# Kernel tuning notes

Measured on AMD Instinct MI355X. Metric: run time of the kernel, lower is better.

## Reference

```python
import jax, jax.numpy as jnp
import numpy as np

B, H, W, C = 16, 56, 56, 256
K = 3          # ikernel
G = 8          # group
C4 = C // 4    # ratio=4
EPS = 1e-5


def setup_inputs() -> dict:
    key = jax.random.key(0)
    ks = jax.random.split(key, 16)
    s = lambda *sh: 1.0 / np.sqrt(sh[-1])
    inp = {
        'x': jax.random.normal(ks[0], (B, H, W, C), jnp.float32),
        # Involution: conv1 (C->C4, 1x1), BN affine, conv2 (C4 -> G*K*K, 1x1)
        'conv1_w': jax.random.normal(ks[1], (C4, C), jnp.float32) * s(C4, C),
        'conv1_b': jnp.zeros((C4,), jnp.float32),
        'bn_gamma': jnp.ones((C4,), jnp.float32),
        'bn_beta': jnp.zeros((C4,), jnp.float32),
        'conv2_w': jax.random.normal(ks[2], (G * K * K, C4), jnp.float32) * s(G * K * K, C4),
        'conv2_b': jnp.zeros((G * K * K,), jnp.float32),
        # mlp_c: Linear(dim, dim, bias=False)
        'mlp_c_w': jax.random.normal(ks[3], (C, C), jnp.float32) * s(C, C),
        # reweight1: Mlp(dim, dim//4, dim*2)
        'fc1_w': jax.random.normal(ks[4], (C4, C), jnp.float32) * s(C4, C),
        'fc1_b': jnp.zeros((C4,), jnp.float32),
        'fc2_w': jax.random.normal(ks[5], (2 * C, C4), jnp.float32) * s(2 * C, C4),
        'fc2_b': jnp.zeros((2 * C,), jnp.float32),
        # projcnn: Conv2d(dim, dim, 1)
        'projcnn_w': jax.random.normal(ks[6], (C, C), jnp.float32) * s(C, C),
        'projcnn_b': jnp.zeros((C,), jnp.float32),
    }
    return inp


def _involution(x, conv1_w, conv1_b, bn_gamma, bn_beta, conv2_w, conv2_b):
    # x: [B,H,W,C] (channels-last equivalent of the torch NCHW path)
    # kernel-generating branch: 1x1 conv -> BN (batch stats, training mode) -> relu -> 1x1 conv
    t = jnp.einsum('bhwc,oc->bhwo', x, conv1_w) + conv1_b          # [B,H,W,C4]
    mu = t.mean(axis=(0, 1, 2))
    var = t.var(axis=(0, 1, 2))
    t = jax.nn.relu(bn_gamma * (t - mu) * jax.lax.rsqrt(var + EPS) + bn_beta)
    w = jnp.einsum('bhwc,oc->bhwo', t, conv2_w) + conv2_b          # [B,H,W,G*K*K]
    w = w.reshape(B, H, W, G, K * K)
    # unfold: pad and stack the K*K shifted views (row-major kernel order, matches torch)
    p = K // 2
    xp = jnp.pad(x, ((0, 0), (p, p), (p, p), (0, 0)))
    patches = jnp.stack([xp[:, i:i + H, j:j + W, :] for i in range(K) for j in range(K)],
                        axis=3)                                     # [B,H,W,KK,C]
    patches = patches.reshape(B, H, W, K * K, G, C // G)
    out = jnp.einsum('bhwkgc,bhwgk->bhwgc', patches, w)             # multiply + sum over kernel dim
    return out.reshape(B, H, W, C)


def reference(x, conv1_w, conv1_b, bn_gamma, bn_beta, conv2_w, conv2_b,
              mlp_c_w, fc1_w, fc1_b, fc2_w, fc2_b, projcnn_w, projcnn_b):
    hw = _involution(x, conv1_w, conv1_b, bn_gamma, bn_beta, conv2_w, conv2_b)  # [B,H,W,C]
    c = jnp.einsum('bhwc,oc->bhwo', x, mlp_c_w)                                  # [B,H,W,C]
    a = (hw + c).mean(axis=(1, 2))                                               # [B,C]
    a = jax.nn.gelu(jnp.einsum('bc,oc->bo', a, fc1_w) + fc1_b, approximate=False)
    a = jnp.einsum('bc,oc->bo', a, fc2_w) + fc2_b                                # [B,2C]
    a = a.reshape(B, C, 2).transpose(2, 0, 1)                                    # [2,B,C]
    a = jax.nn.softmax(a, axis=0)[:, :, None, None, :]                           # [2,B,1,1,C]
    y = hw * a[0] + c * a[1]
    return jnp.einsum('bhwc,oc->bhwo', y, projcnn_w) + projcnn_b
```

## Files before the change

### kernel.cpp

```cpp
#include <hip/hip_runtime.h>
#include <math.h>

#define BB 16
#define HH 56
#define WW 56
#define CC 256
#define O2P 80
#define NPIX 50176
#define HWP 3136

typedef __attribute__((ext_vector_type(4))) float f32x4;
typedef __attribute__((ext_vector_type(8))) short bh8;
typedef __attribute__((ext_vector_type(4))) short bh4;

__device__ inline short f2bf(float f) {
    union { float f; unsigned u; } v; v.f = f;
    unsigned r = (v.u + 0x7fffu + ((v.u >> 16) & 1u)) >> 16;
    return (short)r;
}
__device__ inline float bf2f(short s) {
    union { unsigned u; float f; } v; v.u = ((unsigned)(unsigned short)s) << 16;
    return v.f;
}

__device__ inline void stage_tile(const short* __restrict__ src, int rowBase, int ldk,
                                  int kc, char* smem, int nchunks, int wid, int lane)
{
    for (int ci = wid; ci < nchunks; ci += 4) {
        int row = ci * 8 + (lane >> 3);
        int cb = (lane & 7) ^ (row & 7);
        const short* gp = src + (size_t)(rowBase + row) * ldk + kc + cb * 8;
        __builtin_amdgcn_global_load_lds(
            (const __attribute__((address_space(1))) void*)gp,
            (__attribute__((address_space(3))) void*)(smem + ci * 1024), 16, 0, 0);
    }
}

template<int BN, int AMODE, int OUTBF>
__global__ __launch_bounds__(256) void mgemm(
    const short* __restrict__ Ab,
    const short* __restrict__ At, const float* __restrict__ scsh,
    const short* __restrict__ Ah, const short* __restrict__ Ac,
    const float* __restrict__ g0, const float* __restrict__ g1,
    const short* __restrict__ Wb, const float* __restrict__ bias,
    void* __restrict__ outp, int K, int O, int ldOut)
{
    constexpr int WN = (BN == 128) ? 2 : 1;
    constexpr int MR = (BN == 128) ? 4 : 2;
    constexpr int NR = BN / (16 * WN);
    constexpr int BCH = BN / 8;

    __shared__ alignas(16) char smA[16384];
    __shared__ alignas(16) char smB[BN * 128];

    const int tid = threadIdx.x;
    const int lane = tid & 63, wid = tid >> 6;
    const int rowBase = blockIdx.x * 128;
    const int ocBase = blockIdx.y * BN;
    const int waveM = (BN == 128) ? (wid >> 1) * 64 : wid * 32;
    const int waveN = (BN == 128) ? (wid & 1) * 64 : 0;

    f32x4 acc[MR][NR];
    #pragma unroll
    for (int m = 0; m < MR; ++m)
        #pragma unroll
        for (int n = 0; n < NR; ++n) acc[m][n] = f32x4{0.f, 0.f, 0.f, 0.f};

    for (int kc = 0; kc < K; kc += 64) {
        if constexpr (AMODE == 0) {
            stage_tile(Ab, rowBase, K, kc, smA, 16, wid, lane);
        } else if constexpr (AMODE == 1) {
            #pragma unroll
            for (int q = tid; q < 1024; q += 256) {
                int row = q >> 3, cb = q & 7;
                bh8 v = *(const bh8*)(At + (size_t)(rowBase + row) * K + kc + cb * 8);
                bh8 o;
                #pragma unroll
                for (int j = 0; j < 8; ++j) {
                    int k = kc + cb * 8 + j;
                    o[j] = f2bf(fmaxf(bf2f(v[j]) * scsh[k] + scsh[64 + k], 0.f));
                }
                *(bh8*)(smA + row * 128 + ((cb ^ (row & 7)) << 4)) = o;
            }
        } else {
            #pragma unroll
            for (int q = tid; q < 1024; q += 256) {
                int row = q >> 3, cb = q & 7;
                int n = rowBase + row;
                int b = n / HWP;
                const size_t off = (size_t)n * 256 + kc + cb * 8;
                bh8 h8 = *(const bh8*)(Ah + off);
                bh8 c8 = *(const bh8*)(Ac + off);
                bh8 o;
                #pragma unroll
                for (int j = 0; j < 8; ++j) {
                    float w0 = g0[b * 256 + kc + cb * 8 + j];
                    float w1 = g1[b * 256 + kc + cb * 8 + j];
                    o[j] = f2bf(bf2f(h8[j]) * w0 + bf2f(c8[j]) * w1);
                }
                *(bh8*)(smA + row * 128 + ((cb ^ (row & 7)) << 4)) = o;
            }
        }
        stage_tile(Wb, ocBase, K, kc, smB, BCH, wid, lane);
        __syncthreads();

        #pragma unroll
        for (int ks = 0; ks < 2; ++ks) {
            bh8 aF[MR], bF[NR];
            #pragma unroll
            for (int m = 0; m < MR; ++m) {
                int r = waveM + m * 16 + (lane & 15);
                int cb = ks * 4 + (lane >> 4);
                aF[m] = *(const bh8*)(smA + r * 128 + ((cb ^ (r & 7)) << 4));
            }
            #pragma unroll
            for (int n = 0; n < NR; ++n) {
                int r = waveN + n * 16 + (lane & 15);
                int cb = ks * 4 + (lane >> 4);
                bF[n] = *(const bh8*)(smB + r * 128 + ((cb ^ (r & 7)) << 4));
            }
            #pragma unroll
            for (int m = 0; m < MR; ++m)
                #pragma unroll
                for (int n = 0; n < NR; ++n)
                    acc[m][n] = __builtin_amdgcn_mfma_f32_16x16x32_bf16(
                        aF[m], bF[n], acc[m][n], 0, 0, 0);
        }
        __syncthreads();
    }

    #pragma unroll
    for (int m = 0; m < MR; ++m)
        #pragma unroll
        for (int n = 0; n < NR; ++n)
            #pragma unroll
            for (int j = 0; j < 4; ++j) {
                int r = rowBase + waveM + m * 16 + (lane >> 4) * 4 + j;
                int c = ocBase + waveN + n * 16 + (lane & 15);
                if (c < O) {
                    float v = acc[m][n][j] + (bias ? bias[c] : 0.f);
                    if constexpr (OUTBF)
                        ((short*)outp)[(size_t)r * ldOut + c] = f2bf(v);
                    else
                        ((float*)outp)[(size_t)r * ldOut + c] = v;
                }
            }
}

__global__ __launch_bounds__(256) void cvt_x_kernel(const float* __restrict__ x,
                                                    short* __restrict__ xb,
                                                    float* __restrict__ sxb)
{
    __shared__ float sm[8][256];
    const int tid = threadIdx.x;
    size_t base = (size_t)blockIdx.x * 2048 + tid * 8;
    const int b = (int)(base >> 8) / HWP;
    const int ch0 = (int)(base & 255);
    const int pix = (tid * 8) >> 8;

    f32x4 v0 = *(const f32x4*)(x + base);
    f32x4 v1 = *(const f32x4*)(x + base + 4);
    bh8 o;
    #pragma unroll
    for (int j = 0; j < 4; ++j) { o[j] = f2bf(v0[j]); o[4 + j] = f2bf(v1[j]); }
    *(bh8*)(xb + base) = o;

    #pragma unroll
    for (int j = 0; j < 4; ++j) {
        sm[pix][ch0 + j] = v0[j];
        sm[pix][ch0 + 4 + j] = v1[j];
    }
    __syncthreads();
    float s = 0.f;
    #pragma unroll
    for (int p = 0; p < 8; ++p) s += sm[p][tid];
    atomicAdd(&sxb[b * CC + tid], s);
}

__global__ __launch_bounds__(256) void cvt_w_kernel(
    const float* __restrict__ c1, const float* __restrict__ mc,
    const float* __restrict__ pj, const float* __restrict__ c2,
    short* __restrict__ c1b, short* __restrict__ mcb,
    short* __restrict__ pjb, short* __restrict__ c2b)
{
    int i = blockIdx.x * 256 + threadIdx.x;
    if (i < 16384) c1b[i] = f2bf(c1[i]);
    if (i < 65536) { mcb[i] = f2bf(mc[i]); pjb[i] = f2bf(pj[i]); }
    if (i < O2P * 64) {
        int o = i >> 6, k = i & 63;
        c2b[i] = (o < 72) ? f2bf(c2[o * 64 + k]) : (short)0;
    }
}

__global__ __launch_bounds__(256) void bn_stats_kernel(
    const short* __restrict__ t, float* __restrict__ stats)
{
    __shared__ float ss[32][64], sq[32][64];
    const int tid = threadIdx.x;
    const int grp = tid >> 3, ch0 = (tid & 7) * 8;
    const size_t rowBase = (size_t)blockIdx.x * 512;
    float s[8] = {}, q[8] = {};
    for (int r = grp; r < 512; r += 32) {
        bh8 v = *(const bh8*)(t + (rowBase + r) * 64 + ch0);
        #pragma unroll
        for (int j = 0; j < 8; ++j) {
            float f = bf2f(v[j]);
            s[j] += f; q[j] += f * f;
        }
    }
    #pragma unroll
    for (int j = 0; j < 8; ++j) { ss[grp][ch0 + j] = s[j]; sq[grp][ch0 + j] = q[j]; }
    __syncthreads();
    if (tid < 64) {
        float ts = 0.f, tq = 0.f;
        #pragma unroll
        for (int g = 0; g < 32; ++g) { ts += ss[g][tid]; tq += sq[g][tid]; }
        atomicAdd(&stats[tid], ts);
        atomicAdd(&stats[64 + tid], tq);
    }
}

__global__ void bn_finalize_kernel(
    const float* __restrict__ stats, const float* __restrict__ gamma,
    const float* __restrict__ beta, float* __restrict__ scsh)
{
    int ch = threadIdx.x;
    const float invN = 1.f / (float)NPIX;
    float mean = stats[ch] * invN;
    float var  = stats[64 + ch] * invN - mean * mean;
    float sc = gamma[ch] * rsqrtf(var + 1e-5f);
    scsh[ch] = sc;
    scsh[64 + ch] = beta[ch] - mean * sc;
}

__global__ __launch_bounds__(256) void invol_kernel(
    const short* __restrict__ xb, const short* __restrict__ wmatb,
    short* __restrict__ hwb, float* __restrict__ asum)
{
    __shared__ float sm4[4][256];
    const int idx = blockIdx.x;
    const int s = idx & 1, bh = idx >> 1;
    const int b = bh / HH, h = bh % HH;
    const int tid = threadIdx.x;
    const int lane = tid & 63, wid = tid >> 6;
    const int c4 = lane * 4;
    const int g = lane >> 3;
    const int w0 = s * 28 + wid * 7;
    const short* xbase = xb + ((size_t)b * HWP) * CC + c4;

    float cL[3][4], cM[3][4], cR[3][4];
    auto loadcol = [&](int Wc, float d[3][4]) {
        #pragma unroll
        for (int i = 0; i < 3; ++i) {
            int hh = h + i - 1;
            if (Wc < 0 || Wc >= WW || hh < 0 || hh >= HH) {
                d[i][0] = d[i][1] = d[i][2] = d[i][3] = 0.f;
            } else {
                bh4 v = *(const bh4*)(xbase + (size_t)(hh * WW + Wc) * CC);
                #pragma unroll
                for (int j = 0; j < 4; ++j) d[i][j] = bf2f(v[j]);
            }
        }
    };
    loadcol(w0 - 1, cL);
    loadcol(w0, cM);

    float loc[4] = {0.f, 0.f, 0.f, 0.f};
    for (int w = w0; w < w0 + 7; ++w) {
        loadcol(w + 1, cR);
        const int n = bh * WW + w;
        const short* wr = wmatb + (size_t)n * O2P + g * 9;
        float wf[9];
        #pragma unroll
        for (int t9 = 0; t9 < 9; ++t9) wf[t9] = bf2f(wr[t9]);
        bh4 ov;
        #pragma unroll
        for (int j = 0; j < 4; ++j) {
            float a = cL[0][j] * wf[0] + cM[0][j] * wf[1] + cR[0][j] * wf[2]
                    + cL[1][j] * wf[3] + cM[1][j] * wf[4] + cR[1][j] * wf[5]
                    + cL[2][j] * wf[6] + cM[2][j] * wf[7] + cR[2][j] * wf[8];
            loc[j] += a;
            ov[j] = f2bf(a);
        }
        *(bh4*)(hwb + (size_t)n * CC + c4) = ov;
        #pragma unroll
        for (int i = 0; i < 3; ++i)
            #pragma unroll
            for (int j = 0; j < 4; ++j) { cL[i][j] = cM[i][j]; cM[i][j] = cR[i][j]; }
    }
    #pragma unroll
    for (int j = 0; j < 4; ++j) sm4[wid][c4 + j] = loc[j];
    __syncthreads();
    float tot = sm4[0][tid] + sm4[1][tid] + sm4[2][tid] + sm4[3][tid];
    atomicAdd(&asum[b * CC + tid], tot);
}

__global__ __launch_bounds__(256) void mlp_kernel(
    const float* __restrict__ asum, const float* __restrict__ sxb,
    const float* __restrict__ mlp_c_w,
    const float* __restrict__ fc1_w, const float* __restrict__ fc1_b,
    const float* __restrict__ fc2_w, const float* __restrict__ fc2_b,
    float* __restrict__ a0, float* __restrict__ a1)
{
    __shared__ float a[256], hbuf[64], f[512];
    const int b = blockIdx.x, tid = threadIdx.x;
    float acm = 0.f;
    const float* wrow = mlp_c_w + (size_t)tid * 256;
    for (int c = 0; c < 256; ++c) acm += sxb[b * CC + c] * wrow[c];
    a[tid] = (asum[b * CC + tid] + acm) * (1.f / (float)HWP);
    __syncthreads();
    if (tid < 64) {
        float s = fc1_b[tid];
        for (int c = 0; c < 256; ++c) s += a[c] * fc1_w[tid * 256 + c];
        hbuf[tid] = 0.5f * s * (1.f + erff(s * 0.7071067811865476f));
    }
    __syncthreads();
    for (int o = tid; o < 512; o += 256) {
        float s = fc2_b[o];
        for (int c = 0; c < 64; ++c) s += hbuf[c] * fc2_w[o * 64 + c];
        f[o] = s;
    }
    __syncthreads();
    float f0 = f[2 * tid], f1 = f[2 * tid + 1];
    float m = fmaxf(f0, f1);
    float e0 = expf(f0 - m), e1 = expf(f1 - m);
    float inv = 1.f / (e0 + e1);
    a0[b * CC + tid] = e0 * inv;
    a1[b * CC + tid] = e1 * inv;
}

extern "C" void kernel_launch(void* const* d_in, const int* in_sizes, int n_in,
                              void* d_out, int out_size, void* d_ws, size_t ws_size,
                              hipStream_t stream)
{
    (void)in_sizes; (void)n_in; (void)out_size; (void)ws_size;
    const float* x        = (const float*)d_in[0];
    const float* conv1_w  = (const float*)d_in[1];
    const float* conv1_b  = (const float*)d_in[2];
    const float* bn_gamma = (const float*)d_in[3];
    const float* bn_beta  = (const float*)d_in[4];
    const float* conv2_w  = (const float*)d_in[5];
    const float* conv2_b  = (const float*)d_in[6];
    const float* mlp_c_w  = (const float*)d_in[7];
    const float* fc1_w    = (const float*)d_in[8];
    const float* fc1_b    = (const float*)d_in[9];
    const float* fc2_w    = (const float*)d_in[10];
    const float* fc2_b    = (const float*)d_in[11];
    const float* projcnn_w= (const float*)d_in[12];
    const float* projcnn_b= (const float*)d_in[13];
    float* out = (float*)d_out;

    char* p = (char*)d_ws;
    short* xb  = (short*)p; p += (size_t)NPIX * 256 * 2;
    short* hwb = (short*)p; p += (size_t)NPIX * 256 * 2;
    short* cmb = (short*)p;
    short* t   = (short*)cmb;
    p += (size_t)NPIX * 256 * 2;
    short* wmatb = (short*)p; p += (size_t)NPIX * O2P * 2;
    short* c1b = (short*)p; p += 64 * 256 * 2;
    short* mcb = (short*)p; p += 256 * 256 * 2;
    short* pjb = (short*)p; p += 256 * 256 * 2;
    short* c2b = (short*)p; p += O2P * 64 * 2;
    float* stats = (float*)p; p += 128 * 4;
    float* asum  = (float*)p; p += BB * 256 * 4;
    float* sxb   = (float*)p; p += BB * 256 * 4;
    float* scsh  = (float*)p; p += 128 * 4;
    float* a0    = (float*)p; p += BB * 256 * 4;
    float* a1    = (float*)p; p += BB * 256 * 4;

    hipMemsetAsync(stats, 0, (128 + 2 * BB * 256) * sizeof(float), stream);

    cvt_x_kernel<<<NPIX * 256 / 2048, 256, 0, stream>>>(x, xb, sxb);
    cvt_w_kernel<<<256, 256, 0, stream>>>(conv1_w, mlp_c_w, projcnn_w, conv2_w,
                                          c1b, mcb, pjb, c2b);
    mgemm<64, 0, 1><<<dim3(392, 1), 256, 0, stream>>>(
        xb, nullptr, nullptr, nullptr, nullptr, nullptr, nullptr,
        c1b, conv1_b, t, 256, 64, 64);
    bn_stats_kernel<<<98, 256, 0, stream>>>(t, stats);
    bn_finalize_kernel<<<1, 64, 0, stream>>>(stats, bn_gamma, bn_beta, scsh);
    mgemm<O2P, 1, 1><<<dim3(392, 1), 256, 0, stream>>>(
        nullptr, t, scsh, nullptr, nullptr, nullptr, nullptr,
        c2b, conv2_b, wmatb, 64, 72, O2P);
    invol_kernel<<<BB * HH * 2, 256, 0, stream>>>(xb, wmatb, hwb, asum);
    mgemm<128, 0, 1><<<dim3(392, 2), 256, 0, stream>>>(
        xb, nullptr, nullptr, nullptr, nullptr, nullptr, nullptr,
        mcb, nullptr, cmb, 256, 256, 256);
    mlp_kernel<<<BB, 256, 0, stream>>>(asum, sxb, mlp_c_w,
                                       fc1_w, fc1_b, fc2_w, fc2_b, a0, a1);
    mgemm<128, 2, 0><<<dim3(392, 2), 256, 0, stream>>>(
        nullptr, nullptr, nullptr, hwb, cmb, a0, a1,
        pjb, projcnn_b, out, 256, 256, 256);
}
```

Baseline: 296.4 us.

## Fold softmax gates into per-batch projection weights and shrink GEMM row tiles

```diff
diff --git a/kernel.cpp b/kernel.cpp
--- a/kernel.cpp
+++ b/kernel.cpp
@@ -37,28 +37,29 @@
 }
 
 template<int BN, int AMODE, int OUTBF>
-__global__ __launch_bounds__(256) void mgemm(
-    const short* __restrict__ Ab,
-    const short* __restrict__ At, const float* __restrict__ scsh,
-    const short* __restrict__ Ah, const short* __restrict__ Ac,
-    const float* __restrict__ g0, const float* __restrict__ g1,
+__global__ __launch_bounds__(256) void mgemm64(
+    const short* __restrict__ Ab, const short* __restrict__ A2,
+    const float* __restrict__ scsh,
     const short* __restrict__ Wb, const float* __restrict__ bias,
     void* __restrict__ outp, int K, int O, int ldOut)
 {
-    constexpr int WN = (BN == 128) ? 2 : 1;
-    constexpr int MR = (BN == 128) ? 4 : 2;
-    constexpr int NR = BN / (16 * WN);
+    constexpr int MR = (BN == 80) ? 1 : 2;
+    constexpr int NR = (BN == 80) ? 5 : (BN == 128 ? 4 : 2);
     constexpr int BCH = BN / 8;
 
-    __shared__ alignas(16) char smA[16384];
+    __shared__ alignas(16) char smA[8192];
     __shared__ alignas(16) char smB[BN * 128];
 
     const int tid = threadIdx.x;
     const int lane = tid & 63, wid = tid >> 6;
-    const int rowBase = blockIdx.x * 128;
+    const int rowBase = blockIdx.x * 64;
     const int ocBase = blockIdx.y * BN;
-    const int waveM = (BN == 128) ? (wid >> 1) * 64 : wid * 32;
-    const int waveN = (BN == 128) ? (wid & 1) * 64 : 0;
+    const int waveM = (BN == 80) ? wid * 16 : (wid & 1) * 32;
+    const int waveN = (BN == 80) ? 0 : (BN == 128 ? (wid >> 1) * 64 : (wid >> 1) * 32);
+
+    const short* wptr = Wb;
+    if constexpr (AMODE == 3)
+        wptr += (size_t)(rowBase / HWP) * 256 * 512;
 
     f32x4 acc[MR][NR];
     #pragma unroll
@@ -68,12 +69,15 @@
 
     for (int kc = 0; kc < K; kc += 64) {
         if constexpr (AMODE == 0) {
-            stage_tile(Ab, rowBase, K, kc, smA, 16, wid, lane);
-        } else if constexpr (AMODE == 1) {
-            #pragma unroll
-            for (int q = tid; q < 1024; q += 256) {
+            stage_tile(Ab, rowBase, K, kc, smA, 8, wid, lane);
+        } else if constexpr (AMODE == 3) {
+            const short* s = (kc < 256) ? Ab : A2;
+            stage_tile(s, rowBase, 256, kc & 255, smA, 8, wid, lane);
+        } else {
+            #pragma unroll
+            for (int q = tid; q < 512; q += 256) {
                 int row = q >> 3, cb = q & 7;
-                bh8 v = *(const bh8*)(At + (size_t)(rowBase + row) * K + kc + cb * 8);
+                bh8 v = *(const bh8*)(Ab + (size_t)(rowBase + row) * K + kc + cb * 8);
                 bh8 o;
                 #pragma unroll
                 for (int j = 0; j < 8; ++j) {
@@ -82,26 +86,8 @@
                 }
                 *(bh8*)(smA + row * 128 + ((cb ^ (row & 7)) << 4)) = o;
             }
-        } else {
-            #pragma unroll
-            for (int q = tid; q < 1024; q += 256) {
-                int row = q >> 3, cb = q & 7;
-                int n = rowBase + row;
-                int b = n / HWP;
-                const size_t off = (size_t)n * 256 + kc + cb * 8;
-                bh8 h8 = *(const bh8*)(Ah + off);
-                bh8 c8 = *(const bh8*)(Ac + off);
-                bh8 o;
-                #pragma unroll
-                for (int j = 0; j < 8; ++j) {
-                    float w0 = g0[b * 256 + kc + cb * 8 + j];
-                    float w1 = g1[b * 256 + kc + cb * 8 + j];
-                    o[j] = f2bf(bf2f(h8[j]) * w0 + bf2f(c8[j]) * w1);
-                }
-                *(bh8*)(smA + row * 128 + ((cb ^ (row & 7)) << 4)) = o;
-            }
-        }
-        stage_tile(Wb, ocBase, K, kc, smB, BCH, wid, lane);
+        }
+        stage_tile(wptr, ocBase, K, kc, smB, BCH, wid, lane);
         __syncthreads();
 
         #pragma unroll
@@ -179,17 +165,32 @@
 
 __global__ __launch_bounds__(256) void cvt_w_kernel(
     const float* __restrict__ c1, const float* __restrict__ mc,
-    const float* __restrict__ pj, const float* __restrict__ c2,
-    short* __restrict__ c1b, short* __restrict__ mcb,
-    short* __restrict__ pjb, short* __restrict__ c2b)
+    const float* __restrict__ c2,
+    short* __restrict__ c1b, short* __restrict__ mcb, short* __restrict__ c2b)
 {
     int i = blockIdx.x * 256 + threadIdx.x;
     if (i < 16384) c1b[i] = f2bf(c1[i]);
-    if (i < 65536) { mcb[i] = f2bf(mc[i]); pjb[i] = f2bf(pj[i]); }
+    if (i < 65536) mcb[i] = f2bf(mc[i]);
     if (i < O2P * 64) {
         int o = i >> 6, k = i & 63;
         c2b[i] = (o < 72) ? f2bf(c2[o * 64 + k]) : (short)0;
     }
+}
+
+__global__ __launch_bounds__(256) void fold_w_kernel(
+    const float* __restrict__ pjw, const float* __restrict__ a0,
+    const float* __restrict__ a1, short* __restrict__ wf)
+{
+    size_t base = ((size_t)blockIdx.x * 256 + threadIdx.x) * 8;
+    int b = (int)(base >> 17);
+    int rem = (int)(base & 131071);
+    int o = rem >> 9, k0 = rem & 511;
+    const float* av = (k0 < 256) ? (a0 + b * 256 + k0) : (a1 + b * 256 + k0 - 256);
+    const float* wrow = pjw + o * 256 + (k0 & 255);
+    bh8 ov;
+    #pragma unroll
+    for (int j = 0; j < 8; ++j) ov[j] = f2bf(wrow[j] * av[j]);
+    *(bh8*)(wf + base) = ov;
 }
 
 __global__ __launch_bounds__(256) void bn_stats_kernel(
@@ -305,19 +306,36 @@
     __shared__ float a[256], hbuf[64], f[512];
     const int b = blockIdx.x, tid = threadIdx.x;
     float acm = 0.f;
-    const float* wrow = mlp_c_w + (size_t)tid * 256;
-    for (int c = 0; c < 256; ++c) acm += sxb[b * CC + c] * wrow[c];
+    {
+        const f32x4* w4 = (const f32x4*)(mlp_c_w + (size_t)tid * 256);
+        const f32x4* s4 = (const f32x4*)(sxb + b * CC);
+        for (int c = 0; c < 64; ++c) {
+            f32x4 sv = s4[c], wv = w4[c];
+            acm += sv[0] * wv[0] + sv[1] * wv[1] + sv[2] * wv[2] + sv[3] * wv[3];
+        }
+    }
     a[tid] = (asum[b * CC + tid] + acm) * (1.f / (float)HWP);
     __syncthreads();
     if (tid < 64) {
         float s = fc1_b[tid];
-        for (int c = 0; c < 256; ++c) s += a[c] * fc1_w[tid * 256 + c];
+        const f32x4* w4 = (const f32x4*)(fc1_w + (size_t)tid * 256);
+        const f32x4* a4 = (const f32x4*)a;
+        for (int c = 0; c < 64; ++c) {
+            f32x4 av = a4[c], wv = w4[c];
+            s += av[0] * wv[0] + av[1] * wv[1] + av[2] * wv[2] + av[3] * wv[3];
+        }
         hbuf[tid] = 0.5f * s * (1.f + erff(s * 0.7071067811865476f));
     }
     __syncthreads();
     for (int o = tid; o < 512; o += 256) {
         float s = fc2_b[o];
-        for (int c = 0; c < 64; ++c) s += hbuf[c] * fc2_w[o * 64 + c];
+        const f32x4* w4 = (const f32x4*)(fc2_w + (size_t)o * 64);
+        const f32x4* h4 = (const f32x4*)hbuf;
+        #pragma unroll
+        for (int c = 0; c < 16; ++c) {
+            f32x4 hv = h4[c], wv = w4[c];
+            s += hv[0] * wv[0] + hv[1] * wv[1] + hv[2] * wv[2] + hv[3] * wv[3];
+        }
         f[o] = s;
     }
     __syncthreads();
@@ -357,9 +375,9 @@
     short* t   = (short*)cmb;
     p += (size_t)NPIX * 256 * 2;
     short* wmatb = (short*)p; p += (size_t)NPIX * O2P * 2;
+    short* wfold = (short*)p; p += (size_t)BB * 256 * 512 * 2;
     short* c1b = (short*)p; p += 64 * 256 * 2;
     short* mcb = (short*)p; p += 256 * 256 * 2;
-    short* pjb = (short*)p; p += 256 * 256 * 2;
     short* c2b = (short*)p; p += O2P * 64 * 2;
     float* stats = (float*)p; p += 128 * 4;
     float* asum  = (float*)p; p += BB * 256 * 4;
@@ -371,23 +389,19 @@
     hipMemsetAsync(stats, 0, (128 + 2 * BB * 256) * sizeof(float), stream);
 
     cvt_x_kernel<<<NPIX * 256 / 2048, 256, 0, stream>>>(x, xb, sxb);
-    cvt_w_kernel<<<256, 256, 0, stream>>>(conv1_w, mlp_c_w, projcnn_w, conv2_w,
-                                          c1b, mcb, pjb, c2b);
-    mgemm<64, 0, 1><<<dim3(392, 1), 256, 0, stream>>>(
-        xb, nullptr, nullptr, nullptr, nullptr, nullptr, nullptr,
-        c1b, conv1_b, t, 256, 64, 64);
+    cvt_w_kernel<<<256, 256, 0, stream>>>(conv1_w, mlp_c_w, conv2_w, c1b, mcb, c2b);
+    mgemm64<64, 0, 1><<<dim3(784, 1), 256, 0, stream>>>(
+        xb, nullptr, nullptr, c1b, conv1_b, t, 256, 64, 64);
     bn_stats_kernel<<<98, 256, 0, stream>>>(t, stats);
     bn_finalize_kernel<<<1, 64, 0, stream>>>(stats, bn_gamma, bn_beta, scsh);
-    mgemm<O2P, 1, 1><<<dim3(392, 1), 256, 0, stream>>>(
-        nullptr, t, scsh, nullptr, nullptr, nullptr, nullptr,
-        c2b, conv2_b, wmatb, 64, 72, O2P);
+    mgemm64<O2P, 1, 1><<<dim3(784, 1), 256, 0, stream>>>(
+        t, nullptr, scsh, c2b, conv2_b, wmatb, 64, 72, O2P);
     invol_kernel<<<BB * HH * 2, 256, 0, stream>>>(xb, wmatb, hwb, asum);
-    mgemm<128, 0, 1><<<dim3(392, 2), 256, 0, stream>>>(
-        xb, nullptr, nullptr, nullptr, nullptr, nullptr, nullptr,
-        mcb, nullptr, cmb, 256, 256, 256);
+    mgemm64<128, 0, 1><<<dim3(784, 2), 256, 0, stream>>>(
+        xb, nullptr, nullptr, mcb, nullptr, cmb, 256, 256, 256);
     mlp_kernel<<<BB, 256, 0, stream>>>(asum, sxb, mlp_c_w,
                                        fc1_w, fc1_b, fc2_w, fc2_b, a0, a1);
-    mgemm<128, 2, 0><<<dim3(392, 2), 256, 0, stream>>>(
-        nullptr, nullptr, nullptr, hwb, cmb, a0, a1,
-        pjb, projcnn_b, out, 256, 256, 256);
-}
+    fold_w_kernel<<<1024, 256, 0, stream>>>(projcnn_w, a0, a1, wfold);
+    mgemm64<128, 3, 0><<<dim3(784, 2), 256, 0, stream>>>(
+        hwb, cmb, nullptr, wfold, projcnn_b, out, 512, 256, 256);
+}
```

Measured after the change: 282.0 us. 4.8% less time.
